# Optimization experiments

Hardware: AMD Instinct MI355X
Metric: run time of the kernel (lower is better)

Reference implementation:

```python
import jax, jax.numpy as jnp
import numpy as np

L, B, D = 8192, 4096, 1024


def setup_inputs() -> dict:
    key = jax.random.key(0)
    k1, k2, k3, k4 = jax.random.split(key, 4)
    return {
        "q_hat": jax.random.normal(k1, (L, D), dtype=jnp.float32),
        "q_real": jax.random.normal(k2, (L, D), dtype=jnp.float32),
        "encoded_gt": jax.random.normal(k3, (B, D), dtype=jnp.float32),
        "encoded_pred": jax.random.normal(k4, (B, D), dtype=jnp.float32),
    }


def reference(q_hat, q_real, encoded_gt, encoded_pred):
    # local_loss: -(1/L) * sum_i dot(q_hat[i], q_real[i])
    # (replaces the Python loop of L tiny torch.dot launches with one fused reduce)
    local = -jnp.mean(jnp.sum(q_hat * q_real, axis=-1))

    # global_loss: sum_{i,j} max(0, <pred_i, gt_j> - <pred_i, gt_i> + 1)
    # (replaces the O(B^2) double loop of torch.dot calls with one GEMM)
    scores = jnp.einsum("id,jd->ij", encoded_pred, encoded_gt)  # [B, B]
    pos = jnp.diagonal(scores)                                   # [B]
    margin = jnp.float32(1.0)
    glob = jnp.sum(jnp.maximum(0.0, scores - pos[:, None] + margin))

    return local + glob
```

## Files before the change

### kernel.cpp

```cpp
#include <hip/hip_runtime.h>
#include <hip/hip_bf16.h>

#define LROWS 8192
#define BROWS 4096
#define DDIM  1024

typedef __attribute__((ext_vector_type(4)))  int   i32x4;
typedef __attribute__((ext_vector_type(8)))  int   i32x8;
typedef __attribute__((ext_vector_type(16))) float f32x16;

typedef const unsigned int __attribute__((address_space(1))) gu32;
typedef unsigned int       __attribute__((address_space(3))) su32;

__device__ inline unsigned int pack_fp8x4(float4 v) {
    unsigned int w = 0;
    w = __builtin_amdgcn_cvt_pk_fp8_f32(v.x, v.y, w, false);
    w = __builtin_amdgcn_cvt_pk_fp8_f32(v.z, v.w, w, true);
    return w;
}

__global__ __launch_bounds__(256) void prep_kernel(
    const float4* __restrict__ pred,
    const float4* __restrict__ gt,
    unsigned int* __restrict__ opred,
    unsigned int* __restrict__ ogt,
    float* __restrict__ pos,
    float* __restrict__ out) {
    __shared__ float sred[4];
    const int row = blockIdx.x;
    const int t = threadIdx.x;
    if (row == 0 && t == 0) out[0] = 0.0f;

    const int idx = row * 256 + t;
    float4 p = pred[idx];
    float4 g = gt[idx];
    opred[idx] = pack_fp8x4(p);
    ogt[idx]   = pack_fp8x4(g);
    float s = p.x * g.x + p.y * g.y + p.z * g.z + p.w * g.w;

    #pragma unroll
    for (int o = 32; o > 0; o >>= 1) s += __shfl_down(s, o, 64);
    if ((t & 63) == 0) sred[t >> 6] = s;
    __syncthreads();
    if (t == 0) pos[row] = sred[0] + sred[1] + sred[2] + sred[3];
}

__global__ __launch_bounds__(512, 2) void hinge_gemm(
    const unsigned char* __restrict__ A,
    const unsigned char* __restrict__ Bm,
    const float* __restrict__ pos,
    const float4* __restrict__ qh,
    const float4* __restrict__ qr,
    float* __restrict__ out) {
    extern __shared__ unsigned char smem[];
    unsigned char* const As = smem;
    unsigned char* const Bs = smem + 65536;
    float* const pos_s = (float*)(smem + 131072);
    float* const sred  = (float*)(smem + 132096);
    float* const sred2 = (float*)(smem + 132128);

    const int orig = blockIdx.x;
    const int xk = orig & 7, xj = orig >> 3;
    const int bm = (xk >> 1) * 4 + (xj >> 3);
    const int bn = (xk & 1) * 8 + (xj & 7);

    const int tid = threadIdx.x;
    const int lane = tid & 63;
    const int wave = tid >> 6;
    const int wm = wave >> 2;
    const int wn = wave & 3;

    if (tid < 256) pos_s[tid] = pos[bm * 256 + tid];

    const int grow = lane >> 3;
    const int usw  = (lane & 7) ^ grow;

    const unsigned char* Abase = A  + (size_t)(bm * 256) * DDIM;
    const unsigned char* Bbase = Bm + (size_t)(bn * 256) * DDIM;

    const float4* qhb = qh + (size_t)orig * 8192;
    const float4* qrb = qr + (size_t)orig * 8192;

    f32x16 acc[4][2];
    #pragma unroll
    for (int i = 0; i < 4; i++)
        #pragma unroll
        for (int j = 0; j < 2; j++)
            #pragma unroll
            for (int r = 0; r < 16; r++) acc[i][j][r] = 0.0f;

    const int sc1 = 0x7f7f7f7f;
    const int mrow = lane & 31;
    const int kh = lane >> 5;

    auto stage = [&](int buf, int k0) {
        #pragma unroll
        for (int i = 0; i < 4; i++) {
            const int c = wave * 4 + i;
            const int row = c * 8 + grow;
            __builtin_amdgcn_global_load_lds(
                (gu32*)(Abase + (size_t)row * DDIM + k0 + usw * 16),
                (su32*)(As + buf * 32768 + c * 1024), 16, 0, 0);
            __builtin_amdgcn_global_load_lds(
                (gu32*)(Bbase + (size_t)row * DDIM + k0 + usw * 16),
                (su32*)(Bs + buf * 32768 + c * 1024), 16, 0, 0);
        }
    };

    auto compute = [&](int buf) {
        const unsigned char* Ab = As + buf * 32768;
        const unsigned char* Bb = Bs + buf * 32768;
        #pragma unroll
        for (int h = 0; h < 2; h++) {
            const int u0 = h * 4 + kh * 2;
            i32x8 af[4];
            i32x8 bg[2];
            #pragma unroll
            for (int mt = 0; mt < 4; mt++) {
                const int r = wm * 128 + mt * 32 + mrow;
                i32x4 x0 = *(const i32x4*)&Ab[r * 128 + ((u0    ) ^ (r & 7)) * 16];
                i32x4 x1 = *(const i32x4*)&Ab[r * 128 + ((u0 + 1) ^ (r & 7)) * 16];
                af[mt] = __builtin_shufflevector(x0, x1, 0, 1, 2, 3, 4, 5, 6, 7);
            }
            #pragma unroll
            for (int nt = 0; nt < 2; nt++) {
                const int r = wn * 64 + nt * 32 + mrow;
                i32x4 x0 = *(const i32x4*)&Bb[r * 128 + ((u0    ) ^ (r & 7)) * 16];
                i32x4 x1 = *(const i32x4*)&Bb[r * 128 + ((u0 + 1) ^ (r & 7)) * 16];
                bg[nt] = __builtin_shufflevector(x0, x1, 0, 1, 2, 3, 4, 5, 6, 7);
            }
            __builtin_amdgcn_s_setprio(1);
            #pragma unroll
            for (int mt = 0; mt < 4; mt++)
                #pragma unroll
                for (int nt = 0; nt < 2; nt++)
                    acc[mt][nt] = __builtin_amdgcn_mfma_scale_f32_32x32x64_f8f6f4(
                        af[mt], bg[nt], acc[mt][nt],
                        0, 0,
                        0, sc1,
                        0, sc1);
            __builtin_amdgcn_s_setprio(0);
        }
    };

    float ls = 0.0f;
    float4 ch0, ch1, cr0, cr1;
    float4 nh0, nh1, nr0, nr1;

    stage(0, 0);
    ch0 = qhb[tid];       ch1 = qhb[tid + 512];
    cr0 = qrb[tid];       cr1 = qrb[tid + 512];
    __syncthreads();
    int p = 0;
    for (int t = 0; t < 7; t++) {
        stage(p ^ 1, (t + 1) * 128);
        const int qo = (t + 1) * 1024 + tid;
        nh0 = qhb[qo];       nh1 = qhb[qo + 512];
        nr0 = qrb[qo];       nr1 = qrb[qo + 512];
        ls += ch0.x * cr0.x + ch0.y * cr0.y + ch0.z * cr0.z + ch0.w * cr0.w
            + ch1.x * cr1.x + ch1.y * cr1.y + ch1.z * cr1.z + ch1.w * cr1.w;
        compute(p);
        __syncthreads();
        ch0 = nh0; ch1 = nh1; cr0 = nr0; cr1 = nr1;
        p ^= 1;
    }
    ls += ch0.x * cr0.x + ch0.y * cr0.y + ch0.z * cr0.z + ch0.w * cr0.w
        + ch1.x * cr1.x + ch1.y * cr1.y + ch1.z * cr1.z + ch1.w * cr1.w;
    compute(p);

    float s = 0.0f;
    const int rq = 4 * kh;
    #pragma unroll
    for (int mt = 0; mt < 4; mt++) {
        #pragma unroll
        for (int nt = 0; nt < 2; nt++) {
            #pragma unroll
            for (int i = 0; i < 16; i++) {
                const int lr = wm * 128 + mt * 32 + (i & 3) + 8 * (i >> 2) + rq;
                const float v = acc[mt][nt][i] - pos_s[lr] + 1.0f;
                s += fmaxf(v, 0.0f);
            }
        }
    }
    #pragma unroll
    for (int o = 32; o > 0; o >>= 1) {
        s  += __shfl_down(s, o, 64);
        ls += __shfl_down(ls, o, 64);
    }
    if (lane == 0) { sred[wave] = s; sred2[wave] = ls; }
    __syncthreads();
    if (tid == 0) {
        float tot = 0.0f, lp = 0.0f;
        #pragma unroll
        for (int w = 0; w < 8; w++) { tot += sred[w]; lp += sred2[w]; }
        atomicAdd(out, tot - lp * (1.0f / (float)LROWS));
    }
}

extern "C" void kernel_launch(void* const* d_in, const int* in_sizes, int n_in,
                              void* d_out, int out_size, void* d_ws, size_t ws_size,
                              hipStream_t stream) {
    const float* q_hat  = (const float*)d_in[0];
    const float* q_real = (const float*)d_in[1];
    const float* gt     = (const float*)d_in[2];
    const float* pred   = (const float*)d_in[3];
    float* out = (float*)d_out;

    char* ws = (char*)d_ws;
    unsigned char* pred_8 = (unsigned char*)ws;
    unsigned char* gt_8   = (unsigned char*)(ws + (size_t)BROWS * DDIM);
    float* pos   = (float*)(ws + (size_t)2 * BROWS * DDIM);

    hipLaunchKernelGGL(prep_kernel, dim3(BROWS), dim3(256), 0, stream,
                       (const float4*)pred, (const float4*)gt,
                       (unsigned int*)pred_8, (unsigned int*)gt_8,
                       pos, out);

    const size_t lds_bytes = 131072 + 1024 + 64;
    hipLaunchKernelGGL(hinge_gemm, dim3(256), dim3(512), lds_bytes, stream,
                       pred_8, gt_8, pos,
                       (const float4*)q_hat, (const float4*)q_real, out);
}
```

Measured before the change: 131.2 us.

## Interleave LDS fragment loads, async staging and MFMA in fine-grained barrier-synced phases

Restructures the main K loop into four phases per tile. Each phase reads a slice of A/B fragments, issues one quarter of the next tile's global-to-LDS loads, then runs four MFMAs between explicit s_barriers. Manual s_waitcnt with vmcnt(4) and sched_barriers replace __syncthreads, so the q_hat/q_real register loads can stay in flight while LDS data is waited on. The goal is to overlap memory traffic with matrix math more tightly, at the cost of many more workgroup barriers and fragile hand-managed wait counts.

```diff
diff --git a/kernel.cpp b/kernel.cpp
--- a/kernel.cpp
+++ b/kernel.cpp
@@ -70,8 +70,6 @@
     const int wm = wave >> 2;
     const int wn = wave & 3;
 
-    if (tid < 256) pos_s[tid] = pos[bm * 256 + tid];
-
     const int grow = lane >> 3;
     const int usw  = (lane & 7) ^ grow;
 
@@ -93,18 +91,15 @@
     const int mrow = lane & 31;
     const int kh = lane >> 5;
 
-    auto stage = [&](int buf, int k0) {
-        #pragma unroll
-        for (int i = 0; i < 4; i++) {
-            const int c = wave * 4 + i;
-            const int row = c * 8 + grow;
-            __builtin_amdgcn_global_load_lds(
-                (gu32*)(Abase + (size_t)row * DDIM + k0 + usw * 16),
-                (su32*)(As + buf * 32768 + c * 1024), 16, 0, 0);
-            __builtin_amdgcn_global_load_lds(
-                (gu32*)(Bbase + (size_t)row * DDIM + k0 + usw * 16),
-                (su32*)(Bs + buf * 32768 + c * 1024), 16, 0, 0);
-        }
+    auto stage_one = [&](int buf, int k0, int i) {
+        const int c = wave * 4 + i;
+        const int row = c * 8 + grow;
+        __builtin_amdgcn_global_load_lds(
+            (gu32*)(Abase + (size_t)row * DDIM + k0 + usw * 16),
+            (su32*)(As + buf * 32768 + c * 1024), 16, 0, 0);
+        __builtin_amdgcn_global_load_lds(
+            (gu32*)(Bbase + (size_t)row * DDIM + k0 + usw * 16),
+            (su32*)(Bs + buf * 32768 + c * 1024), 16, 0, 0);
     };
 
     auto compute = [&](int buf) {
@@ -135,10 +130,7 @@
                 #pragma unroll
                 for (int nt = 0; nt < 2; nt++)
                     acc[mt][nt] = __builtin_amdgcn_mfma_scale_f32_32x32x64_f8f6f4(
-                        af[mt], bg[nt], acc[mt][nt],
-                        0, 0,
-                        0, sc1,
-                        0, sc1);
+                        af[mt], bg[nt], acc[mt][nt], 0, 0, 0, sc1, 0, sc1);
             __builtin_amdgcn_s_setprio(0);
         }
     };
@@ -147,26 +139,90 @@
     float4 ch0, ch1, cr0, cr1;
     float4 nh0, nh1, nr0, nr1;
 
-    stage(0, 0);
+    if (tid < 256) pos_s[tid] = pos[bm * 256 + tid];
+    __builtin_amdgcn_sched_barrier(0);
+    #pragma unroll
+    for (int i = 0; i < 4; i++) stage_one(0, 0, i);
+    __builtin_amdgcn_sched_barrier(0);
     ch0 = qhb[tid];       ch1 = qhb[tid + 512];
     cr0 = qrb[tid];       cr1 = qrb[tid + 512];
-    __syncthreads();
+    __builtin_amdgcn_sched_barrier(0);
+    asm volatile("s_waitcnt vmcnt(4) lgkmcnt(0)" ::: "memory");
+    __builtin_amdgcn_sched_barrier(0);
+    __builtin_amdgcn_s_barrier();
+
     int p = 0;
-    for (int t = 0; t < 7; t++) {
-        stage(p ^ 1, (t + 1) * 128);
-        const int qo = (t + 1) * 1024 + tid;
-        nh0 = qhb[qo];       nh1 = qhb[qo + 512];
-        nr0 = qrb[qo];       nr1 = qrb[qo + 512];
-        ls += ch0.x * cr0.x + ch0.y * cr0.y + ch0.z * cr0.z + ch0.w * cr0.w
-            + ch1.x * cr1.x + ch1.y * cr1.y + ch1.z * cr1.z + ch1.w * cr1.w;
-        compute(p);
-        __syncthreads();
+    for (int t = 0; t < 7; ++t) {
+        const int k0n = (t + 1) * 128;
+        const unsigned char* Ab = As + p * 32768;
+        const unsigned char* Bb = Bs + p * 32768;
+        i32x8 bgr0, bgr1;
+        #pragma unroll
+        for (int g = 0; g < 4; ++g) {
+            const int h = g >> 1, half = g & 1;
+            const int u0 = h * 4 + kh * 2;
+            __builtin_amdgcn_sched_barrier(0);
+            if (half == 0) {
+                {
+                    const int r = wn * 64 + mrow;
+                    i32x4 x0 = *(const i32x4*)&Bb[r * 128 + ((u0    ) ^ (r & 7)) * 16];
+                    i32x4 x1 = *(const i32x4*)&Bb[r * 128 + ((u0 + 1) ^ (r & 7)) * 16];
+                    bgr0 = __builtin_shufflevector(x0, x1, 0, 1, 2, 3, 4, 5, 6, 7);
+                }
+                {
+                    const int r = wn * 64 + 32 + mrow;
+                    i32x4 x0 = *(const i32x4*)&Bb[r * 128 + ((u0    ) ^ (r & 7)) * 16];
+                    i32x4 x1 = *(const i32x4*)&Bb[r * 128 + ((u0 + 1) ^ (r & 7)) * 16];
+                    bgr1 = __builtin_shufflevector(x0, x1, 0, 1, 2, 3, 4, 5, 6, 7);
+                }
+            }
+            i32x8 af0, af1;
+            {
+                const int r = wm * 128 + (half * 2) * 32 + mrow;
+                i32x4 x0 = *(const i32x4*)&Ab[r * 128 + ((u0    ) ^ (r & 7)) * 16];
+                i32x4 x1 = *(const i32x4*)&Ab[r * 128 + ((u0 + 1) ^ (r & 7)) * 16];
+                af0 = __builtin_shufflevector(x0, x1, 0, 1, 2, 3, 4, 5, 6, 7);
+            }
+            {
+                const int r = wm * 128 + (half * 2 + 1) * 32 + mrow;
+                i32x4 x0 = *(const i32x4*)&Ab[r * 128 + ((u0    ) ^ (r & 7)) * 16];
+                i32x4 x1 = *(const i32x4*)&Ab[r * 128 + ((u0 + 1) ^ (r & 7)) * 16];
+                af1 = __builtin_shufflevector(x0, x1, 0, 1, 2, 3, 4, 5, 6, 7);
+            }
+            stage_one(p ^ 1, k0n, g);
+            if (g == 3) {
+                __builtin_amdgcn_sched_barrier(0);
+                ls += ch0.x * cr0.x + ch0.y * cr0.y + ch0.z * cr0.z + ch0.w * cr0.w
+                    + ch1.x * cr1.x + ch1.y * cr1.y + ch1.z * cr1.z + ch1.w * cr1.w;
+                const int qo = (t + 1) * 1024 + tid;
+                nh0 = qhb[qo];       nh1 = qhb[qo + 512];
+                nr0 = qrb[qo];       nr1 = qrb[qo + 512];
+            }
+            __builtin_amdgcn_sched_barrier(0);
+            __builtin_amdgcn_s_barrier();
+            __builtin_amdgcn_sched_barrier(0);
+            __builtin_amdgcn_s_setprio(1);
+            acc[half * 2][0] = __builtin_amdgcn_mfma_scale_f32_32x32x64_f8f6f4(
+                af0, bgr0, acc[half * 2][0], 0, 0, 0, sc1, 0, sc1);
+            acc[half * 2][1] = __builtin_amdgcn_mfma_scale_f32_32x32x64_f8f6f4(
+                af0, bgr1, acc[half * 2][1], 0, 0, 0, sc1, 0, sc1);
+            acc[half * 2 + 1][0] = __builtin_amdgcn_mfma_scale_f32_32x32x64_f8f6f4(
+                af1, bgr0, acc[half * 2 + 1][0], 0, 0, 0, sc1, 0, sc1);
+            acc[half * 2 + 1][1] = __builtin_amdgcn_mfma_scale_f32_32x32x64_f8f6f4(
+                af1, bgr1, acc[half * 2 + 1][1], 0, 0, 0, sc1, 0, sc1);
+            __builtin_amdgcn_s_setprio(0);
+            if (g == 3) {
+                asm volatile("s_waitcnt vmcnt(4)" ::: "memory");
+            }
+            __builtin_amdgcn_sched_barrier(0);
+            __builtin_amdgcn_s_barrier();
+        }
         ch0 = nh0; ch1 = nh1; cr0 = nr0; cr1 = nr1;
         p ^= 1;
     }
+    compute(p);
     ls += ch0.x * cr0.x + ch0.y * cr0.y + ch0.z * cr0.z + ch0.w * cr0.w
         + ch1.x * cr1.x + ch1.y * cr1.y + ch1.z * cr1.z + ch1.w * cr1.w;
-    compute(p);
 
     float s = 0.0f;
     const int rq = 4 * kh;
```

After: 131.4 us. About the same (+0.2%).

## Shrink GEMM tiles to 128x128 with two waves and single-buffered LDS

Applied to the files above, without the earlier changes.

Moves the hinge GEMM from 256x256 tiles with 8 waves and double-buffered LDS to 128x128 tiles with 2 waves, 1024 blocks and a single LDS buffer. Block-to-tile mapping is reworked so each XCD holds a contiguous band of A rows. The aim is more blocks and more blocks resident per CU from the lower LDS use, for better load balance. The cost is lost overlap between global loads and MFMA, since each step now loads and then waits on barriers, plus more global traffic from less reuse per tile.

```diff
diff --git a/kernel.cpp b/kernel.cpp
--- a/kernel.cpp
+++ b/kernel.cpp
@@ -45,7 +45,7 @@
     if (t == 0) pos[row] = sred[0] + sred[1] + sred[2] + sred[3];
 }
 
-__global__ __launch_bounds__(512, 2) void hinge_gemm(
+__global__ __launch_bounds__(128, 2) void hinge_gemm(
     const unsigned char* __restrict__ A,
     const unsigned char* __restrict__ Bm,
     const float* __restrict__ pos,
@@ -54,32 +54,29 @@
     float* __restrict__ out) {
     extern __shared__ unsigned char smem[];
     unsigned char* const As = smem;
-    unsigned char* const Bs = smem + 65536;
-    float* const pos_s = (float*)(smem + 131072);
-    float* const sred  = (float*)(smem + 132096);
-    float* const sred2 = (float*)(smem + 132128);
+    unsigned char* const Bs = smem + 16384;
+    float* const pos_s = (float*)(smem + 32768);
+    float* const sred  = (float*)(smem + 33280);
+    float* const sred2 = (float*)(smem + 33288);
 
     const int orig = blockIdx.x;
-    const int xk = orig & 7, xj = orig >> 3;
-    const int bm = (xk >> 1) * 4 + (xj >> 3);
-    const int bn = (xk & 1) * 8 + (xj & 7);
+    const int xcd = orig & 7, idx = orig >> 3;
+    const int bm = xcd * 4 + (idx & 3);
+    const int bn = idx >> 2;
 
     const int tid = threadIdx.x;
     const int lane = tid & 63;
     const int wave = tid >> 6;
-    const int wm = wave >> 2;
-    const int wn = wave & 3;
-
-    if (tid < 256) pos_s[tid] = pos[bm * 256 + tid];
+    const int wn = wave;
 
     const int grow = lane >> 3;
     const int usw  = (lane & 7) ^ grow;
 
-    const unsigned char* Abase = A  + (size_t)(bm * 256) * DDIM;
-    const unsigned char* Bbase = Bm + (size_t)(bn * 256) * DDIM;
-
-    const float4* qhb = qh + (size_t)orig * 8192;
-    const float4* qrb = qr + (size_t)orig * 8192;
+    const unsigned char* Abase = A  + (size_t)(bm * 128) * DDIM;
+    const unsigned char* Bbase = Bm + (size_t)(bn * 128) * DDIM;
+
+    const float4* qhb = qh + (size_t)orig * 2048;
+    const float4* qrb = qr + (size_t)orig * 2048;
 
     f32x16 acc[4][2];
     #pragma unroll
@@ -93,23 +90,23 @@
     const int mrow = lane & 31;
     const int kh = lane >> 5;
 
-    auto stage = [&](int buf, int k0) {
-        #pragma unroll
-        for (int i = 0; i < 4; i++) {
-            const int c = wave * 4 + i;
+    if (tid < 128) pos_s[tid] = pos[bm * 128 + tid];
+
+    auto stage = [&](int k0) {
+        #pragma unroll
+        for (int i = 0; i < 8; i++) {
+            const int c = wave * 8 + i;
             const int row = c * 8 + grow;
             __builtin_amdgcn_global_load_lds(
                 (gu32*)(Abase + (size_t)row * DDIM + k0 + usw * 16),
-                (su32*)(As + buf * 32768 + c * 1024), 16, 0, 0);
+                (su32*)(As + c * 1024), 16, 0, 0);
             __builtin_amdgcn_global_load_lds(
                 (gu32*)(Bbase + (size_t)row * DDIM + k0 + usw * 16),
-                (su32*)(Bs + buf * 32768 + c * 1024), 16, 0, 0);
+                (su32*)(Bs + c * 1024), 16, 0, 0);
         }
     };
 
-    auto compute = [&](int buf) {
-        const unsigned char* Ab = As + buf * 32768;
-        const unsigned char* Bb = Bs + buf * 32768;
+    auto compute = [&]() {
         #pragma unroll
         for (int h = 0; h < 2; h++) {
             const int u0 = h * 4 + kh * 2;
@@ -117,16 +114,16 @@
             i32x8 bg[2];
             #pragma unroll
             for (int mt = 0; mt < 4; mt++) {
-                const int r = wm * 128 + mt * 32 + mrow;
-                i32x4 x0 = *(const i32x4*)&Ab[r * 128 + ((u0    ) ^ (r & 7)) * 16];
-                i32x4 x1 = *(const i32x4*)&Ab[r * 128 + ((u0 + 1) ^ (r & 7)) * 16];
+                const int r = mt * 32 + mrow;
+                i32x4 x0 = *(const i32x4*)&As[r * 128 + ((u0    ) ^ (r & 7)) * 16];
+                i32x4 x1 = *(const i32x4*)&As[r * 128 + ((u0 + 1) ^ (r & 7)) * 16];
                 af[mt] = __builtin_shufflevector(x0, x1, 0, 1, 2, 3, 4, 5, 6, 7);
             }
             #pragma unroll
             for (int nt = 0; nt < 2; nt++) {
                 const int r = wn * 64 + nt * 32 + mrow;
-                i32x4 x0 = *(const i32x4*)&Bb[r * 128 + ((u0    ) ^ (r & 7)) * 16];
-                i32x4 x1 = *(const i32x4*)&Bb[r * 128 + ((u0 + 1) ^ (r & 7)) * 16];
+                i32x4 x0 = *(const i32x4*)&Bs[r * 128 + ((u0    ) ^ (r & 7)) * 16];
+                i32x4 x1 = *(const i32x4*)&Bs[r * 128 + ((u0 + 1) ^ (r & 7)) * 16];
                 bg[nt] = __builtin_shufflevector(x0, x1, 0, 1, 2, 3, 4, 5, 6, 7);
             }
             __builtin_amdgcn_s_setprio(1);
@@ -135,10 +132,7 @@
                 #pragma unroll
                 for (int nt = 0; nt < 2; nt++)
                     acc[mt][nt] = __builtin_amdgcn_mfma_scale_f32_32x32x64_f8f6f4(
-                        af[mt], bg[nt], acc[mt][nt],
-                        0, 0,
-                        0, sc1,
-                        0, sc1);
+                        af[mt], bg[nt], acc[mt][nt], 0, 0, 0, sc1, 0, sc1);
             __builtin_amdgcn_s_setprio(0);
         }
     };
@@ -146,27 +140,23 @@
     float ls = 0.0f;
     float4 ch0, ch1, cr0, cr1;
     float4 nh0, nh1, nr0, nr1;
-
-    stage(0, 0);
-    ch0 = qhb[tid];       ch1 = qhb[tid + 512];
-    cr0 = qrb[tid];       cr1 = qrb[tid + 512];
-    __syncthreads();
-    int p = 0;
-    for (int t = 0; t < 7; t++) {
-        stage(p ^ 1, (t + 1) * 128);
-        const int qo = (t + 1) * 1024 + tid;
-        nh0 = qhb[qo];       nh1 = qhb[qo + 512];
-        nr0 = qrb[qo];       nr1 = qrb[qo + 512];
+    ch0 = qhb[tid];       ch1 = qhb[tid + 128];
+    cr0 = qrb[tid];       cr1 = qrb[tid + 128];
+
+    for (int t = 0; t < 8; t++) {
+        stage(t * 128);
+        if (t < 7) {
+            const int qo = (t + 1) * 256 + tid;
+            nh0 = qhb[qo];       nh1 = qhb[qo + 128];
+            nr0 = qrb[qo];       nr1 = qrb[qo + 128];
+        }
         ls += ch0.x * cr0.x + ch0.y * cr0.y + ch0.z * cr0.z + ch0.w * cr0.w
             + ch1.x * cr1.x + ch1.y * cr1.y + ch1.z * cr1.z + ch1.w * cr1.w;
-        compute(p);
+        __syncthreads();
+        compute();
         __syncthreads();
         ch0 = nh0; ch1 = nh1; cr0 = nr0; cr1 = nr1;
-        p ^= 1;
-    }
-    ls += ch0.x * cr0.x + ch0.y * cr0.y + ch0.z * cr0.z + ch0.w * cr0.w
-        + ch1.x * cr1.x + ch1.y * cr1.y + ch1.z * cr1.z + ch1.w * cr1.w;
-    compute(p);
+    }
 
     float s = 0.0f;
     const int rq = 4 * kh;
@@ -176,7 +166,7 @@
         for (int nt = 0; nt < 2; nt++) {
             #pragma unroll
             for (int i = 0; i < 16; i++) {
-                const int lr = wm * 128 + mt * 32 + (i & 3) + 8 * (i >> 2) + rq;
+                const int lr = mt * 32 + (i & 3) + 8 * (i >> 2) + rq;
                 const float v = acc[mt][nt][i] - pos_s[lr] + 1.0f;
                 s += fmaxf(v, 0.0f);
             }
@@ -190,10 +180,8 @@
     if (lane == 0) { sred[wave] = s; sred2[wave] = ls; }
     __syncthreads();
     if (tid == 0) {
-        float tot = 0.0f, lp = 0.0f;
-        #pragma unroll
-        for (int w = 0; w < 8; w++) { tot += sred[w]; lp += sred2[w]; }
-        atomicAdd(out, tot - lp * (1.0f / (float)LROWS));
+        atomicAdd(out, sred[0] + sred[1]
+                       - (sred2[0] + sred2[1]) * (1.0f / (float)LROWS));
     }
 }
 
@@ -216,8 +204,8 @@
                        (unsigned int*)pred_8, (unsigned int*)gt_8,
                        pos, out);
 
-    const size_t lds_bytes = 131072 + 1024 + 64;
-    hipLaunchKernelGGL(hinge_gemm, dim3(256), dim3(512), lds_bytes, stream,
+    const size_t lds_bytes = 32768 + 512 + 16;
+    hipLaunchKernelGGL(hinge_gemm, dim3(1024), dim3(128), lds_bytes, stream,
                        pred_8, gt_8, pos,
                        (const float4*)q_hat, (const float4*)q_real, out);
 }
```

Measured after the change: 157.5 us. 20.0% more time.
